# Performance work log

Hardware: AMD Instinct MI355X
Metric: run time of the kernel (lower is better)

Reference implementation:

```python
import jax, jax.numpy as jnp
import numpy as np

RADIUS = 0.1
NSAMPLE = 32


def setup_inputs() -> dict:
    key = jax.random.key(0)
    k1, k2, k3, k4, k5 = jax.random.split(key, 5)
    B, NPOINT, N, C = 4, 2048, 8192, 64
    query_xyz = jax.random.uniform(k1, (B, 3, NPOINT), dtype=jnp.float32)
    support_xyz = jax.random.uniform(k2, (B, 3, N), dtype=jnp.float32)
    query_mask = jax.random.bernoulli(k3, 0.9, (B, NPOINT))
    support_mask = jax.random.bernoulli(k4, 0.9, (B, N))
    features = jax.random.normal(k5, (B, C, N), dtype=jnp.float32)
    return {"query_xyz": query_xyz, "support_xyz": support_xyz,
            "query_mask": query_mask, "support_mask": support_mask,
            "features": features}


def _masked_ordered_ball_query(query_xyz, support_xyz, query_mask, support_mask,
                               radius, nsample):
    # query_xyz: (B,3,npoint), support_xyz: (B,3,N)
    q = query_xyz.transpose(0, 2, 1)    # (B, npoint, 3)
    s = support_xyz.transpose(0, 2, 1)  # (B, N, 3)
    N = s.shape[1]
    # squared pairwise distances via |q|^2 + |s|^2 - 2 q.s  -> (B, npoint, N)
    d2 = (jnp.sum(q * q, -1)[:, :, None]
          + jnp.sum(s * s, -1)[:, None, :]
          - 2.0 * jnp.einsum('bpd,bnd->bpn', q, s))
    within = (d2 <= radius * radius) \
        & support_mask[:, None, :] & query_mask[:, :, None]
    # ordered selection of the first `nsample` in-ball indices (ascending index)
    score = jnp.where(within, N - jnp.arange(N, dtype=jnp.int32), 0)
    vals, idx = jax.lax.top_k(score, nsample)     # (B, npoint, nsample)
    idx_mask = vals > 0                            # true neighbors
    # pad slots with the first found neighbor (0 if none found)
    first = jnp.where(idx_mask[..., :1], idx[..., :1], 0)
    idx = jnp.where(idx_mask, idx, first)
    return idx, idx_mask


def _group(points_nc, idx):
    # points_nc: (B, N, D), idx: (B, npoint, nsample) -> (B, npoint, nsample, D)
    return jax.vmap(lambda p, i: p[i])(points_nc, idx)


def reference(query_xyz, support_xyz, query_mask, support_mask, features):
    idx, idx_mask = _masked_ordered_ball_query(
        query_xyz, support_xyz, query_mask, support_mask, RADIUS, NSAMPLE)
    s = support_xyz.transpose(0, 2, 1)             # (B, N, 3)
    grouped_xyz = _group(s, idx).transpose(0, 3, 1, 2)   # (B,3,npoint,nsample)
    grouped_xyz = grouped_xyz - query_xyz[:, :, :, None]
    grouped_xyz = grouped_xyz / RADIUS             # normalize_xyz=True
    f = features.transpose(0, 2, 1)                # (B, N, C)
    grouped_features = _group(f, idx).transpose(0, 3, 1, 2)  # (B,C,npoint,nsample)
    new_features = jnp.concatenate([grouped_xyz, grouped_features], axis=1)
    return new_features, idx_mask
```

## Files before the change

### kernel.cpp

```cpp
#include <hip/hip_runtime.h>


#define NPOINT 2048
#define NSUP   8192
#define NCH    64
#define NS     32
#define GRID1  10
#define CELLS  1000
#define QCHUNK 1024

__device__ __forceinline__ bool probe_mask4(const void* mask) {
    const unsigned char* mb = (const unsigned char*)mask;
    const int lane = threadIdx.x & 63;
    return __ballot(mb[4 * lane + 1] != 0) == 0ull;
}
__device__ __forceinline__ bool read_mask(const void* mask, int i, bool is4) {
    return is4 ? (((const int*)mask)[i] != 0)
               : (((const unsigned char*)mask)[i] != 0);
}
__device__ __forceinline__ int cell_of(float x, float y, float z) {
    const int cx = min(GRID1 - 1, (int)(x * 10.0f));
    const int cy = min(GRID1 - 1, (int)(y * 10.0f));
    const int cz = min(GRID1 - 1, (int)(z * 10.0f));
    return cx + GRID1 * cy + GRID1 * GRID1 * cz;
}

__global__ __launch_bounds__(256) void zero_ws(int* __restrict__ ptr, int n) {
    const int i = blockIdx.x * 256 + threadIdx.x;
    if (i < n) ptr[i] = 0;
}

__global__ __launch_bounds__(256) void grid_hist(
    const float* __restrict__ support_xyz, const void* __restrict__ support_mask,
    int* __restrict__ starts)
{
    const bool m4 = probe_mask4(support_mask);
    const int gid = blockIdx.x * 256 + threadIdx.x;
    const int b = gid / NSUP, n = gid % NSUP;
    if (!read_mask(support_mask, gid, m4)) return;
    const float* sx = support_xyz + (size_t)b * 3 * NSUP;
    const int cid = cell_of(sx[n], sx[NSUP + n], sx[2 * NSUP + n]);
    atomicAdd(&starts[b * (CELLS + 1) + cid + 1], 1);
}

__global__ __launch_bounds__(1024) void grid_scan(int* __restrict__ starts) {
    __shared__ int scanb[1024];
    const int tid = threadIdx.x;
    int* sb = starts + blockIdx.x * (CELLS + 1);
    scanb[tid] = (tid < CELLS) ? sb[tid + 1] : 0;
    __syncthreads();
    for (int d = 1; d < 1024; d <<= 1) {
        int v = 0;
        if (tid >= d) v = scanb[tid - d];
        __syncthreads();
        if (tid >= d) scanb[tid] += v;
        __syncthreads();
    }
    if (tid < CELLS) sb[tid + 1] = scanb[tid];
}

__global__ __launch_bounds__(256) void grid_fill(
    const float* __restrict__ support_xyz, const void* __restrict__ support_mask,
    const int* __restrict__ starts, int* __restrict__ cursors,
    float4* __restrict__ pts)
{
    const bool m4 = probe_mask4(support_mask);
    const int gid = blockIdx.x * 256 + threadIdx.x;
    const int b = gid / NSUP, n = gid % NSUP;
    if (!read_mask(support_mask, gid, m4)) return;
    const float* sx = support_xyz + (size_t)b * 3 * NSUP;
    const float x = sx[n], y = sx[NSUP + n], z = sx[2 * NSUP + n];
    const int cid = cell_of(x, y, z);
    const int pos = starts[b * (CELLS + 1) + cid]
                  + atomicAdd(&cursors[b * CELLS + cid], 1);
    pts[(size_t)b * NSUP + pos] = make_float4(x, y, z, __int_as_float(n));
}

__global__ __launch_bounds__(256) void mqag_query(
    const float* __restrict__ query_xyz, const float* __restrict__ support_xyz,
    const void* __restrict__ query_mask, const void* __restrict__ support_mask,
    const float4* __restrict__ pts, const int* __restrict__ starts,
    int* __restrict__ idx_ws, float* __restrict__ out, int B)
{
#pragma clang fp contract(off)
    const int wib  = threadIdx.x >> 6;
    const int lane = threadIdx.x & 63;
    const int qid  = blockIdx.x * 4 + wib;
    const int b    = qid / NPOINT;
    const int p    = qid % NPOINT;

    __shared__ int hits_all[4][64];
    __shared__ int slots_all[4][NS];
    int* hits  = hits_all[wib];
    int* slots = slots_all[wib];

    const bool m4s = probe_mask4(support_mask);
    const bool m4q = probe_mask4(query_mask);

    const float* sx = support_xyz + (size_t)b * 3 * NSUP;
    const float* sy = sx + NSUP;
    const float* sz = sx + 2 * NSUP;

    const float qx = query_xyz[(size_t)b * 3 * NPOINT + p];
    const float qy = query_xyz[(size_t)b * 3 * NPOINT + NPOINT + p];
    const float qz = query_xyz[(size_t)b * 3 * NPOINT + 2 * NPOINT + p];
    const bool  qm = read_mask(query_mask, b * NPOINT + p, m4q);
    const float qq = (qx * qx + qy * qy) + qz * qz;

    int cnt = 0;
    if (qm) {
        const int x0 = max(0, (int)floorf((qx - 0.101f) * 10.f));
        const int x1 = min(GRID1 - 1, (int)floorf((qx + 0.101f) * 10.f));
        const int y0 = max(0, (int)floorf((qy - 0.101f) * 10.f));
        const int y1 = min(GRID1 - 1, (int)floorf((qy + 0.101f) * 10.f));
        const int z0 = max(0, (int)floorf((qz - 0.101f) * 10.f));
        const int z1 = min(GRID1 - 1, (int)floorf((qz + 0.101f) * 10.f));
        const int ncx = x1 - x0 + 1;

        const int*    stb  = starts + b * (CELLS + 1);
        const float4* ptsb = pts + (size_t)b * NSUP;

        for (int cz = z0; cz <= z1; ++cz) {
            for (int cy = y0; cy <= y1; ++cy) {
                const int c0 = x0 + GRID1 * cy + GRID1 * GRID1 * cz;
                const int s0 = stb[c0];
                const int e0 = stb[c0 + ncx];
                for (int tb = s0; tb < e0; tb += 64) {
                    const int g  = tb + lane;
                    const bool valid = g < e0;
                    const float4 pv = ptsb[valid ? g : (e0 - 1)];
                    const int nidx = __float_as_int(pv.w);
                    const float ss  = (pv.x * pv.x + pv.y * pv.y) + pv.z * pv.z;
                    const float dot = __builtin_fmaf(qz, pv.z,
                                      __builtin_fmaf(qy, pv.y, qx * pv.x));
                    const float d2  = (qq + ss) - 2.0f * dot;
                    const bool within = valid && (d2 <= 0.01f)
                        && read_mask(support_mask, b * NSUP + nidx, m4s);
                    const unsigned long long bal = __ballot(within);
                    if (within) {
                        const int r = cnt + __popcll(bal & ((1ull << lane) - 1ull));
                        if (r < 64) hits[r] = nidx;
                    }
                    cnt += __popcll(bal);
                }
            }
        }
    }

    __syncthreads();

    if (cnt > 64) {
        int c2 = 0;
        for (int basei = 0; basei < NSUP; basei += 64) {
            const int n = basei + lane;
            const float x = sx[n], y = sy[n], z = sz[n];
            const bool  m = read_mask(support_mask, b * NSUP + n, m4s);
            const float ss  = (x * x + y * y) + z * z;
            const float dot = __builtin_fmaf(qz, z,
                              __builtin_fmaf(qy, y, qx * x));
            const float d2  = (qq + ss) - 2.0f * dot;
            const bool within = (d2 <= 0.01f) && m;
            const unsigned long long bal = __ballot(within);
            if (within) {
                const int r = c2 + __popcll(bal & ((1ull << lane) - 1ull));
                if (r < NS) slots[r] = n;
            }
            c2 += __popcll(bal);
            if (c2 >= NS) break;
        }
        cnt = c2;
    } else {
        int v = (lane < cnt) ? hits[lane] : 0x7FFFFFFF;
        #pragma unroll
        for (int k = 2; k <= 64; k <<= 1) {
            #pragma unroll
            for (int j = k >> 1; j > 0; j >>= 1) {
                const int pv = __shfl_xor(v, j, 64);
                const bool keep_min = ((lane & j) == 0) == ((lane & k) == 0);
                const int mn = min(v, pv), mx = max(v, pv);
                v = keep_min ? mn : mx;
            }
        }
        if (lane < NS && lane < cnt) slots[lane] = v;
    }
    const int found = (cnt < NS) ? cnt : NS;

    __syncthreads();
    const int first = (found > 0) ? slots[0] : 0;
    if (lane < NS && lane >= found) slots[lane] = first;
    __syncthreads();

    if (lane < NS) idx_ws[((size_t)b * NPOINT + p) * NS + lane] = slots[lane];

    const size_t nf_elems = (size_t)B * 67 * NPOINT * NS;
    if (lane < NS) {
        out[nf_elems + ((size_t)b * NPOINT + p) * NS + lane] =
            (lane < found) ? 1.0f : 0.0f;
    }

    for (int i = 0; i < 2; ++i) {
        const int flat = i * 64 + lane;
        if (flat < 3 * NS) {
            const int ch = flat >> 5;
            const int k  = flat & 31;
            const int idx = slots[k];
            const float s = sx[(size_t)ch * NSUP + idx];
            const float q = (ch == 0) ? qx : ((ch == 1) ? qy : qz);
            out[(((size_t)b * 67 + ch) * NPOINT + p) * NS + k] = (s - q) / 0.1f;
        }
    }
}

__global__ __launch_bounds__(256) void gather_feat(
    const float* __restrict__ features, const int* __restrict__ idx_ws,
    float* __restrict__ out, int B)
{
    __shared__ float row[NSUP];
    const int bc = blockIdx.y;
    const int b  = bc / NCH, ch = bc % NCH;
    const int p0 = blockIdx.x * QCHUNK;

    const float* src = features + ((size_t)b * NCH + ch) * NSUP;
    const float4* src4 = (const float4*)src;
    for (int i = threadIdx.x; i < NSUP / 4; i += 256)
        ((float4*)row)[i] = src4[i];
    __syncthreads();

    const int4* idx4 = (const int4*)(idx_ws + ((size_t)b * NPOINT + p0) * NS);
    float4* dst4 = (float4*)(out + (((size_t)b * 67 + 3 + ch) * NPOINT + p0) * NS);
    for (int e = threadIdx.x; e < QCHUNK * NS / 4; e += 256) {
        const int4 iv = idx4[e];
        dst4[e] = make_float4(row[iv.x], row[iv.y], row[iv.z], row[iv.w]);
    }
}

__global__ __launch_bounds__(256) void mqag_linear(
    const float* __restrict__ query_xyz, const float* __restrict__ support_xyz,
    const void* __restrict__ query_mask_raw, const void* __restrict__ support_mask_raw,
    const float* __restrict__ features, float* __restrict__ out, int B)
{
#pragma clang fp contract(off)
    const int wib  = threadIdx.x >> 6;
    const int lane = threadIdx.x & 63;
    const int qid  = blockIdx.x * 4 + wib;
    const int b    = qid / NPOINT;
    const int p    = qid % NPOINT;

    __shared__ int slots_all[4][NS];
    int* slots = slots_all[wib];

    const bool m4s = probe_mask4(support_mask_raw);
    const bool m4q = probe_mask4(query_mask_raw);

    const float* sx = support_xyz + (size_t)b * 3 * NSUP;
    const float* sy = sx + NSUP;
    const float* sz = sx + 2 * NSUP;

    const float qx = query_xyz[(size_t)b * 3 * NPOINT + p];
    const float qy = query_xyz[(size_t)b * 3 * NPOINT + NPOINT + p];
    const float qz = query_xyz[(size_t)b * 3 * NPOINT + 2 * NPOINT + p];
    const bool  qm = read_mask(query_mask_raw, b * NPOINT + p, m4q);
    const float qq = (qx * qx + qy * qy) + qz * qz;

    int cnt = 0;
    if (qm) {
        for (int base = 0; base < NSUP; base += 64) {
            const int n = base + lane;
            const float x = sx[n], y = sy[n], z = sz[n];
            const bool  m = read_mask(support_mask_raw, b * NSUP + n, m4s);
            const float ss  = (x * x + y * y) + z * z;
            const float dot = __builtin_fmaf(qz, z, __builtin_fmaf(qy, y, qx * x));
            const float d2  = (qq + ss) - 2.0f * dot;
            const bool within = (d2 <= 0.01f) && m;
            const unsigned long long bal = __ballot(within);
            if (within) {
                const int r = cnt + __popcll(bal & ((1ull << lane) - 1ull));
                if (r < NS) slots[r] = n;
            }
            cnt += __popcll(bal);
            if (cnt >= NS) break;
        }
    }
    const int found = cnt < NS ? cnt : NS;
    __syncthreads();
    const int first = (found > 0) ? slots[0] : 0;
    if (lane < NS && lane >= found) slots[lane] = first;
    __syncthreads();

    const size_t nf_elems = (size_t)B * 67 * NPOINT * NS;
    if (lane < NS) {
        out[nf_elems + ((size_t)b * NPOINT + p) * NS + lane] =
            (lane < found) ? 1.0f : 0.0f;
    }
    const float* feat = features + (size_t)b * NCH * NSUP;
    for (int i = 0; i < (67 * NS + 63) / 64; ++i) {
        const int flat = i * 64 + lane;
        if (flat < 67 * NS) {
            const int ch = flat >> 5;
            const int k  = flat & 31;
            const int idx = slots[k];
            float val;
            if (ch < 3) {
                const float s = sx[(size_t)ch * NSUP + idx];
                const float q = (ch == 0) ? qx : ((ch == 1) ? qy : qz);
                val = (s - q) / 0.1f;
            } else {
                val = feat[(size_t)(ch - 3) * NSUP + idx];
            }
            out[(((size_t)b * 67 + ch) * NPOINT + p) * NS + k] = val;
        }
    }
}

extern "C" void kernel_launch(void* const* d_in, const int* in_sizes, int n_in,
                              void* d_out, int out_size, void* d_ws, size_t ws_size,
                              hipStream_t stream) {
    const float* query_xyz    = (const float*)d_in[0];
    const float* support_xyz  = (const float*)d_in[1];
    const void*  query_mask   = d_in[2];
    const void*  support_mask = d_in[3];
    const float* features     = (const float*)d_in[4];

    const int B = in_sizes[0] / (3 * NPOINT);

    const size_t off_pts     = 0;
    const size_t off_starts  = off_pts + (size_t)B * NSUP * sizeof(float4);
    const size_t off_cursors = off_starts + (size_t)B * (CELLS + 1) * sizeof(int);
    const size_t off_idx     = off_cursors + (size_t)B * CELLS * sizeof(int);
    const size_t need = off_idx + (size_t)B * NPOINT * NS * sizeof(int);

    if (ws_size >= need) {
        float4* pts  = (float4*)((char*)d_ws + off_pts);
        int* starts  = (int*)((char*)d_ws + off_starts);
        int* cursors = (int*)((char*)d_ws + off_cursors);
        int* idx_ws  = (int*)((char*)d_ws + off_idx);

        const int nzero = B * (CELLS + 1) + B * CELLS;
        hipLaunchKernelGGL(zero_ws, dim3((nzero + 255) / 256), dim3(256), 0,
                           stream, starts, nzero);
        hipLaunchKernelGGL(grid_hist, dim3(B * NSUP / 256), dim3(256), 0,
                           stream, support_xyz, support_mask, starts);
        hipLaunchKernelGGL(grid_scan, dim3(B), dim3(1024), 0, stream, starts);
        hipLaunchKernelGGL(grid_fill, dim3(B * NSUP / 256), dim3(256), 0,
                           stream, support_xyz, support_mask, starts, cursors, pts);
        hipLaunchKernelGGL(mqag_query, dim3(B * NPOINT / 4), dim3(256), 0,
                           stream, query_xyz, support_xyz, query_mask,
                           support_mask, pts, starts, idx_ws, (float*)d_out, B);
        hipLaunchKernelGGL(gather_feat, dim3(NPOINT / QCHUNK, B * NCH), dim3(256),
                           0, stream, features, idx_ws, (float*)d_out, B);
    } else {
        hipLaunchKernelGGL(mqag_linear, dim3(B * NPOINT / 4), dim3(256), 0,
                           stream, query_xyz, support_xyz, query_mask,
                           support_mask, features, (float*)d_out, B);
    }
}
```

Before: 122.9 us.

## Fuse grid histogram and scan, drop redundant mask check, move xyz gather

Merges the zero, histogram and scan kernels into one per-batch kernel that builds the cell histogram with shared-memory atomics and also clears the cursors. This removes two launches and the global atomics. Drops the support-mask read in the neighbor loop, since masked points are never inserted into the grid. Moves the normalized xyz gather out of the query kernel into the feature gather kernel, which now covers 67 channels and stages the query coordinates in shared memory. The fused histogram runs with only B blocks, so it has low parallelism in exchange for fewer launches.

```diff
diff --git a/kernel.cpp b/kernel.cpp
--- a/kernel.cpp
+++ b/kernel.cpp
@@ -25,29 +25,29 @@
     return cx + GRID1 * cy + GRID1 * GRID1 * cz;
 }
 
-__global__ __launch_bounds__(256) void zero_ws(int* __restrict__ ptr, int n) {
-    const int i = blockIdx.x * 256 + threadIdx.x;
-    if (i < n) ptr[i] = 0;
-}
-
-__global__ __launch_bounds__(256) void grid_hist(
+__global__ __launch_bounds__(1024) void grid_hist_scan(
     const float* __restrict__ support_xyz, const void* __restrict__ support_mask,
-    int* __restrict__ starts)
-{
-    const bool m4 = probe_mask4(support_mask);
-    const int gid = blockIdx.x * 256 + threadIdx.x;
-    const int b = gid / NSUP, n = gid % NSUP;
-    if (!read_mask(support_mask, gid, m4)) return;
-    const float* sx = support_xyz + (size_t)b * 3 * NSUP;
-    const int cid = cell_of(sx[n], sx[NSUP + n], sx[2 * NSUP + n]);
-    atomicAdd(&starts[b * (CELLS + 1) + cid + 1], 1);
-}
-
-__global__ __launch_bounds__(1024) void grid_scan(int* __restrict__ starts) {
+    int* __restrict__ starts, int* __restrict__ cursors)
+{
+    __shared__ int cnt_s[CELLS];
     __shared__ int scanb[1024];
     const int tid = threadIdx.x;
-    int* sb = starts + blockIdx.x * (CELLS + 1);
-    scanb[tid] = (tid < CELLS) ? sb[tid + 1] : 0;
+    const int b   = blockIdx.x;
+    const bool m4 = probe_mask4(support_mask);
+
+    const float* sx = support_xyz + (size_t)b * 3 * NSUP;
+    for (int i = tid; i < CELLS; i += 1024) cnt_s[i] = 0;
+    __syncthreads();
+
+    for (int n = tid; n < NSUP; n += 1024) {
+        if (read_mask(support_mask, b * NSUP + n, m4)) {
+            const int cid = cell_of(sx[n], sx[NSUP + n], sx[2 * NSUP + n]);
+            atomicAdd(&cnt_s[cid], 1);
+        }
+    }
+    __syncthreads();
+
+    scanb[tid] = (tid < CELLS) ? cnt_s[tid] : 0;
     __syncthreads();
     for (int d = 1; d < 1024; d <<= 1) {
         int v = 0;
@@ -56,7 +56,10 @@
         if (tid >= d) scanb[tid] += v;
         __syncthreads();
     }
+    int* sb = starts + b * (CELLS + 1);
+    if (tid == 0) sb[0] = 0;
     if (tid < CELLS) sb[tid + 1] = scanb[tid];
+    for (int i = tid; i < CELLS; i += 1024) cursors[b * CELLS + i] = 0;
 }
 
 __global__ __launch_bounds__(256) void grid_fill(
@@ -134,8 +137,7 @@
                     const float dot = __builtin_fmaf(qz, pv.z,
                                       __builtin_fmaf(qy, pv.y, qx * pv.x));
                     const float d2  = (qq + ss) - 2.0f * dot;
-                    const bool within = valid && (d2 <= 0.01f)
-                        && read_mask(support_mask, b * NSUP + nidx, m4s);
+                    const bool within = valid && (d2 <= 0.01f);
                     const unsigned long long bal = __ballot(within);
                     if (within) {
                         const int r = cnt + __popcll(bal & ((1ull << lane) - 1ull));
@@ -197,41 +199,51 @@
         out[nf_elems + ((size_t)b * NPOINT + p) * NS + lane] =
             (lane < found) ? 1.0f : 0.0f;
     }
-
-    for (int i = 0; i < 2; ++i) {
-        const int flat = i * 64 + lane;
-        if (flat < 3 * NS) {
-            const int ch = flat >> 5;
-            const int k  = flat & 31;
-            const int idx = slots[k];
-            const float s = sx[(size_t)ch * NSUP + idx];
-            const float q = (ch == 0) ? qx : ((ch == 1) ? qy : qz);
-            out[(((size_t)b * 67 + ch) * NPOINT + p) * NS + k] = (s - q) / 0.1f;
-        }
-    }
-}
-
-__global__ __launch_bounds__(256) void gather_feat(
+}
+
+__global__ __launch_bounds__(256) void gather_all(
+    const float* __restrict__ support_xyz, const float* __restrict__ query_xyz,
     const float* __restrict__ features, const int* __restrict__ idx_ws,
     float* __restrict__ out, int B)
 {
     __shared__ float row[NSUP];
+    __shared__ float qrow[QCHUNK];
     const int bc = blockIdx.y;
-    const int b  = bc / NCH, ch = bc % NCH;
+    const int b  = bc / 67, c = bc % 67;
     const int p0 = blockIdx.x * QCHUNK;
-
-    const float* src = features + ((size_t)b * NCH + ch) * NSUP;
+    const bool is_xyz = (c < 3);
+
+    const float* src = is_xyz
+        ? support_xyz + ((size_t)b * 3 + c) * NSUP
+        : features + ((size_t)b * NCH + (c - 3)) * NSUP;
     const float4* src4 = (const float4*)src;
     for (int i = threadIdx.x; i < NSUP / 4; i += 256)
         ((float4*)row)[i] = src4[i];
+    if (is_xyz) {
+        const float* qsrc = query_xyz + ((size_t)b * 3 + c) * NPOINT + p0;
+        for (int i = threadIdx.x; i < QCHUNK; i += 256) qrow[i] = qsrc[i];
+    }
     __syncthreads();
 
     const int4* idx4 = (const int4*)(idx_ws + ((size_t)b * NPOINT + p0) * NS);
-    float4* dst4 = (float4*)(out + (((size_t)b * 67 + 3 + ch) * NPOINT + p0) * NS);
-    for (int e = threadIdx.x; e < QCHUNK * NS / 4; e += 256) {
-        const int4 iv = idx4[e];
-        dst4[e] = make_float4(row[iv.x], row[iv.y], row[iv.z], row[iv.w]);
-    }
+    float4* dst4 = (float4*)(out + (((size_t)b * 67 + c) * NPOINT + p0) * NS);
+    const int iters = QCHUNK * NS / 4 / 256;
+    if (is_xyz) {
+        for (int e = threadIdx.x; e < QCHUNK * NS / 4; e += 256) {
+            const int4 iv = idx4[e];
+            const float q = qrow[e >> 3];
+            dst4[e] = make_float4((row[iv.x] - q) / 0.1f,
+                                  (row[iv.y] - q) / 0.1f,
+                                  (row[iv.z] - q) / 0.1f,
+                                  (row[iv.w] - q) / 0.1f);
+        }
+    } else {
+        for (int e = threadIdx.x; e < QCHUNK * NS / 4; e += 256) {
+            const int4 iv = idx4[e];
+            dst4[e] = make_float4(row[iv.x], row[iv.y], row[iv.z], row[iv.w]);
+        }
+    }
+    (void)iters;
 }
 
 __global__ __launch_bounds__(256) void mqag_linear(
@@ -335,19 +347,16 @@
         int* cursors = (int*)((char*)d_ws + off_cursors);
         int* idx_ws  = (int*)((char*)d_ws + off_idx);
 
-        const int nzero = B * (CELLS + 1) + B * CELLS;
-        hipLaunchKernelGGL(zero_ws, dim3((nzero + 255) / 256), dim3(256), 0,
-                           stream, starts, nzero);
-        hipLaunchKernelGGL(grid_hist, dim3(B * NSUP / 256), dim3(256), 0,
-                           stream, support_xyz, support_mask, starts);
-        hipLaunchKernelGGL(grid_scan, dim3(B), dim3(1024), 0, stream, starts);
+        hipLaunchKernelGGL(grid_hist_scan, dim3(B), dim3(1024), 0, stream,
+                           support_xyz, support_mask, starts, cursors);
         hipLaunchKernelGGL(grid_fill, dim3(B * NSUP / 256), dim3(256), 0,
                            stream, support_xyz, support_mask, starts, cursors, pts);
         hipLaunchKernelGGL(mqag_query, dim3(B * NPOINT / 4), dim3(256), 0,
                            stream, query_xyz, support_xyz, query_mask,
                            support_mask, pts, starts, idx_ws, (float*)d_out, B);
-        hipLaunchKernelGGL(gather_feat, dim3(NPOINT / QCHUNK, B * NCH), dim3(256),
-                           0, stream, features, idx_ws, (float*)d_out, B);
+        hipLaunchKernelGGL(gather_all, dim3(NPOINT / QCHUNK, B * 67), dim3(256),
+                           0, stream, support_xyz, query_xyz, features, idx_ws,
+                           (float*)d_out, B);
     } else {
         hipLaunchKernelGGL(mqag_linear, dim3(B * NPOINT / 4), dim3(256), 0,
                            stream, query_xyz, support_xyz, query_mask,
```

After: 124.2 us. About the same (+1.1%).
